# Performance work log

Measured on AMD Instinct MI355X. Metric: run time of the kernel, lower is better.

The kernel has to match this reference:

```python
import jax, jax.numpy as jnp
import numpy as np

N = 50000
E = 1600000
IN_CH = 128
HID = 32
HEADS = 4
OUT_CH = 1
BN_EPS = 1e-5
NEG_SLOPE = 0.2


def _gat_layer(x, src, dst, W, att_src, att_dst, bias, heads, ch, concat, n_nodes):
    # x: [N, F_in], W: [F_in, heads*ch]
    h = (x @ W).reshape(n_nodes, heads, ch)            # [N, H, C]
    e_src = jnp.einsum('nhc,hc->nh', h, att_src)       # [N, H]
    e_dst = jnp.einsum('nhc,hc->nh', h, att_dst)       # [N, H]
    alpha = jax.nn.leaky_relu(e_src[src] + e_dst[dst], NEG_SLOPE)  # [E, H]
    # segment softmax over incoming edges of each dst node
    m = jax.ops.segment_max(alpha, dst, num_segments=n_nodes)      # [N, H]
    ex = jnp.exp(alpha - m[dst])
    den = jax.ops.segment_sum(ex, dst, num_segments=n_nodes)       # [N, H]
    a = ex / (den[dst] + 1e-16)                                    # [E, H]
    out = jax.ops.segment_sum(a[:, :, None] * h[src], dst, num_segments=n_nodes)  # [N, H, C]
    out = out.reshape(n_nodes, heads * ch) if concat else out.mean(axis=1)
    return out + bias


def _batch_norm(x, gamma, beta):
    mean = x.mean(axis=0)
    var = x.var(axis=0)  # biased, as torch uses for normalization
    return (x - mean) * jax.lax.rsqrt(var + BN_EPS) * gamma + beta


def setup_inputs() -> dict:
    key = jax.random.key(0)
    ks = jax.random.split(key, 16)
    hd = HID * HEADS  # 128
    s = lambda fan: 1.0 / np.sqrt(fan)
    return {
        'x': jax.random.normal(ks[0], (N, IN_CH), dtype=jnp.float32),
        'edge_index': jax.random.randint(ks[1], (2, E), 0, N, dtype=jnp.int64),
        'W1': jax.random.normal(ks[2], (IN_CH, hd), dtype=jnp.float32) * s(IN_CH),
        'a1s': jax.random.normal(ks[3], (HEADS, HID), dtype=jnp.float32) * s(HID),
        'a1d': jax.random.normal(ks[4], (HEADS, HID), dtype=jnp.float32) * s(HID),
        'b1': jnp.zeros((hd,), dtype=jnp.float32),
        'g1': jnp.ones((hd,), dtype=jnp.float32),
        'be1': jnp.zeros((hd,), dtype=jnp.float32),
        'W2': jax.random.normal(ks[5], (hd, hd), dtype=jnp.float32) * s(hd),
        'a2s': jax.random.normal(ks[6], (HEADS, HID), dtype=jnp.float32) * s(HID),
        'a2d': jax.random.normal(ks[7], (HEADS, HID), dtype=jnp.float32) * s(HID),
        'b2': jnp.zeros((hd,), dtype=jnp.float32),
        'g2': jnp.ones((hd,), dtype=jnp.float32),
        'be2': jnp.zeros((hd,), dtype=jnp.float32),
        'W3': jax.random.normal(ks[8], (hd, OUT_CH), dtype=jnp.float32) * s(hd),
        'a3s': jax.random.normal(ks[9], (1, OUT_CH), dtype=jnp.float32),
        'a3d': jax.random.normal(ks[10], (1, OUT_CH), dtype=jnp.float32),
        'b3': jnp.zeros((OUT_CH,), dtype=jnp.float32),
    }


def reference(x, edge_index, W1, a1s, a1d, b1, g1, be1, W2, a2s, a2d, b2, g2, be2, W3, a3s, a3d, b3):
    # add self loops (PyG GATConv default), guarantees every dst has >=1 edge
    loops = jnp.arange(N, dtype=edge_index.dtype)
    src = jnp.concatenate([edge_index[0], loops])
    dst = jnp.concatenate([edge_index[1], loops])

    h = _gat_layer(x, src, dst, W1, a1s, a1d, b1, HEADS, HID, True, N)
    h = jax.nn.relu(_batch_norm(h, g1, be1))
    h = _gat_layer(h, src, dst, W2, a2s, a2d, b2, HEADS, HID, True, N)
    h = jax.nn.relu(_batch_norm(h, g2, be2))
    h = _gat_layer(h, src, dst, W3, a3s, a3d, b3, 1, OUT_CH, True, N)
    return jax.nn.relu(h)
```

## Files before the change

### kernel.cpp

```cpp
#include <hip/hip_runtime.h>
#include <hip/hip_fp16.h>
#include <math.h>

#define NEG_SLOPE 0.2f
#define NBMAX 256
#define CHUNK 2048
#define DCAP 16384
#define NREP 32

typedef _Float16 half8 __attribute__((ext_vector_type(8)));
typedef float f32x4 __attribute__((ext_vector_type(4)));

__device__ __forceinline__ float lrelu(float x) { return x > 0.f ? x : NEG_SLOPE * x; }

__device__ __forceinline__ float h2f(unsigned short u) {
    __half h = *(__half*)&u;
    return __half2float(h);
}

__global__ __launch_bounds__(256) void k_hist(const int* __restrict__ ei, int* __restrict__ bCntR,
                                              int E, int n) {
    __shared__ int lh[NBMAX];
    for (int i = threadIdx.x; i < NBMAX; i += 256) lh[i] = 0;
    __syncthreads();
    int E2 = E + n;
    for (int e = blockIdx.x * 256 + threadIdx.x; e < E2; e += gridDim.x * 256) {
        int d = (e < E) ? ei[E + e] : (e - E);
        atomicAdd(&lh[d >> 8], 1);
    }
    __syncthreads();
    int rep = blockIdx.x & (NREP - 1);
    for (int i = threadIdx.x; i < NBMAX; i += 256)
        if (lh[i]) atomicAdd(&bCntR[rep * NBMAX + i], lh[i]);
}

__global__ __launch_bounds__(256) void k_bscan(const int* __restrict__ bCntR, int* __restrict__ bOff,
                                               int* __restrict__ bFill, int* __restrict__ rowptr,
                                               int n, int E2) {
    int NB = (n + 255) >> 8;
    int tid = threadIdx.x, lane = tid & 63, wid = tid >> 6;
    int v0 = 0, v1 = 0, v2 = 0, v3 = 0;
    #pragma unroll
    for (int r = 0; r < NREP; r += 4) {
        v0 += bCntR[(r + 0) * NBMAX + tid];
        v1 += bCntR[(r + 1) * NBMAX + tid];
        v2 += bCntR[(r + 2) * NBMAX + tid];
        v3 += bCntR[(r + 3) * NBMAX + tid];
    }
    int v = (tid < NB) ? (v0 + v1 + v2 + v3) : 0;
    int s = v;
    #pragma unroll
    for (int off = 1; off < 64; off <<= 1) {
        int t = __shfl_up(s, off);
        if (lane >= off) s += t;
    }
    __shared__ int ws[4];
    if (lane == 63) ws[wid] = s;
    __syncthreads();
    if (tid == 0) {
        int c = 0;
        #pragma unroll
        for (int i = 0; i < 4; ++i) { int t = ws[i]; ws[i] = c; c += t; }
    }
    __syncthreads();
    s += ws[wid];
    int excl = s - v;
    if (tid < NB) { bOff[tid] = excl; bFill[tid] = excl; }
    if (tid == NB - 1) bOff[NB] = excl + v;
    if (tid == 0) rowptr[n] = E2;
}

__global__ __launch_bounds__(256) void k_partition(const int* __restrict__ ei, int* __restrict__ bFill,
                                                   unsigned int* __restrict__ staging, int E, int n) {
    __shared__ int lh[NBMAX];
    __shared__ int lbase[NBMAX];
    int E2 = E + n;
    int beg = blockIdx.x * CHUNK;
    int end = min(beg + CHUNK, E2);
    for (int i = threadIdx.x; i < NBMAX; i += 256) lh[i] = 0;
    __syncthreads();
    for (int e = beg + threadIdx.x; e < end; e += 256) {
        int d = (e < E) ? ei[E + e] : (e - E);
        atomicAdd(&lh[d >> 8], 1);
    }
    __syncthreads();
    for (int i = threadIdx.x; i < NBMAX; i += 256) {
        int c = lh[i];
        lbase[i] = c ? atomicAdd(&bFill[i], c) : 0;
        lh[i] = 0;
    }
    __syncthreads();
    for (int e = beg + threadIdx.x; e < end; e += 256) {
        int s, d;
        if (e < E) { s = ei[e]; d = ei[E + e]; } else { s = d = e - E; }
        int b = d >> 8;
        int r = atomicAdd(&lh[b], 1);
        staging[lbase[b] + r] = ((unsigned)s << 8) | (unsigned)(d & 255);
    }
}

__global__ __launch_bounds__(512) void k_emit(const unsigned int* __restrict__ staging,
                                              const int* __restrict__ bOff, int* __restrict__ rowptr,
                                              int* __restrict__ csr, int n) {
    __shared__ int lcnt[NBMAX];
    __shared__ int lscan[NBMAX];
    __shared__ int ws[4];
    __shared__ int sorted[DCAP];
    int b = blockIdx.x;
    int gbase = b << 8;
    int beg = bOff[b], end = bOff[b + 1], m = end - beg;
    int tid = threadIdx.x, lane = tid & 63, wid = tid >> 6;

    if (tid < 256) lcnt[tid] = 0;
    __syncthreads();
    for (int j = tid; j < m; j += 512) atomicAdd(&lcnt[staging[beg + j] & 255], 1);
    __syncthreads();
    int v = 0, s = 0;
    if (tid < 256) {
        v = lcnt[tid];
        s = v;
        #pragma unroll
        for (int off = 1; off < 64; off <<= 1) {
            int t = __shfl_up(s, off);
            if (lane >= off) s += t;
        }
        if (lane == 63) ws[wid] = s;
    }
    __syncthreads();
    if (tid == 0) {
        int c = 0;
        #pragma unroll
        for (int i = 0; i < 4; ++i) { int t = ws[i]; ws[i] = c; c += t; }
    }
    __syncthreads();
    if (tid < 256) {
        int excl = s + ws[wid] - v;
        lscan[tid] = excl;
        lcnt[tid] = 0;
        if (gbase + tid < n) rowptr[gbase + tid] = beg + excl;
    }
    __syncthreads();

    if (m <= DCAP) {
        for (int j = tid; j < m; j += 512) {
            unsigned e = staging[beg + j];
            int ld = e & 255;
            int src = e >> 8;
            int r = atomicAdd(&lcnt[ld], 1);
            sorted[lscan[ld] + r] = src;
        }
        __syncthreads();
        for (int j = tid; j < m; j += 512) csr[beg + j] = sorted[j];
    } else {
        for (int j = tid; j < m; j += 512) {
            unsigned e = staging[beg + j];
            int ld = e & 255;
            int src = e >> 8;
            int r = atomicAdd(&lcnt[ld], 1);
            csr[beg + lscan[ld] + r] = src;
        }
    }
}

__global__ __launch_bounds__(256) void k_gemm_mfma(
    const float* __restrict__ X, const float* __restrict__ W,
    unsigned short* __restrict__ Hout,
    const float* __restrict__ scale, const float* __restrict__ shift,
    const float* __restrict__ as_f, const float* __restrict__ ad_f,
    float* __restrict__ es, float* __restrict__ ed,
    float* __restrict__ bnzero, int n) {
    __shared__ _Float16 WT[128 * 128];
    int tid = threadIdx.x;
    if (blockIdx.x < NREP) bnzero[blockIdx.x * 256 + tid] = 0.f;

    const float4* W4 = (const float4*)W;
    #pragma unroll
    for (int t = 0; t < 16; ++t) {
        int flat = tid + t * 256;
        int k = flat >> 5;
        int n4 = flat & 31;
        float4 wv = W4[flat];
        int nb = n4 * 4;
        #pragma unroll
        for (int i = 0; i < 4; ++i) {
            int nn = nb + i;
            float val = (i == 0) ? wv.x : (i == 1) ? wv.y : (i == 2) ? wv.z : wv.w;
            int byte = nn * 256 + k * 2;
            byte ^= (nn & 7) << 4;
            *(_Float16*)((char*)WT + byte) = (_Float16)val;
        }
    }
    __syncthreads();

    int wid = tid >> 6, lane = tid & 63;
    int l15 = lane & 15, lg = lane >> 4;
    int row0 = blockIdx.x * 64 + wid * 16;
    int myrow = row0 + l15;
    bool rok = myrow < n;

    f32x4 acc[8];
    #pragma unroll
    for (int i = 0; i < 8; ++i) acc[i] = (f32x4){0.f, 0.f, 0.f, 0.f};

    #pragma unroll
    for (int ks = 0; ks < 4; ++ks) {
        int kb = ks * 32 + lg * 8;
        half8 a;
        #pragma unroll
        for (int j = 0; j < 8; ++j) a[j] = (_Float16)0.f;
        if (rok) {
            float4 x0 = *(const float4*)(X + (size_t)myrow * 128 + kb);
            float4 x1 = *(const float4*)(X + (size_t)myrow * 128 + kb + 4);
            if (scale) {
                float4 sc0 = *(const float4*)&scale[kb], sh0 = *(const float4*)&shift[kb];
                float4 sc1 = *(const float4*)&scale[kb + 4], sh1 = *(const float4*)&shift[kb + 4];
                x0.x = fmaxf(x0.x * sc0.x + sh0.x, 0.f);
                x0.y = fmaxf(x0.y * sc0.y + sh0.y, 0.f);
                x0.z = fmaxf(x0.z * sc0.z + sh0.z, 0.f);
                x0.w = fmaxf(x0.w * sc0.w + sh0.w, 0.f);
                x1.x = fmaxf(x1.x * sc1.x + sh1.x, 0.f);
                x1.y = fmaxf(x1.y * sc1.y + sh1.y, 0.f);
                x1.z = fmaxf(x1.z * sc1.z + sh1.z, 0.f);
                x1.w = fmaxf(x1.w * sc1.w + sh1.w, 0.f);
            }
            a[0] = (_Float16)x0.x; a[1] = (_Float16)x0.y;
            a[2] = (_Float16)x0.z; a[3] = (_Float16)x0.w;
            a[4] = (_Float16)x1.x; a[5] = (_Float16)x1.y;
            a[6] = (_Float16)x1.z; a[7] = (_Float16)x1.w;
        }
        #pragma unroll
        for (int nt = 0; nt < 8; ++nt) {
            int nn = nt * 16 + l15;
            int byte = nn * 256 + kb * 2;
            byte ^= (nn & 7) << 4;
            half8 b = *(const half8*)((const char*)WT + byte);
            acc[nt] = __builtin_amdgcn_mfma_f32_16x16x32_f16(a, b, acc[nt], 0, 0, 0);
        }
    }

    #pragma unroll
    for (int nt = 0; nt < 8; ++nt) {
        #pragma unroll
        for (int r = 0; r < 4; ++r) {
            int rr = row0 + lg * 4 + r;
            if (rr < n) {
                _Float16 hv = (_Float16)acc[nt][r];
                Hout[(size_t)rr * 128 + nt * 16 + l15] = *(unsigned short*)&hv;
            }
        }
    }

    float asv[8], adv[8];
    #pragma unroll
    for (int nt = 0; nt < 8; ++nt) {
        asv[nt] = as_f[nt * 16 + l15];
        adv[nt] = ad_f[nt * 16 + l15];
    }
    float ps[4][4], pd[4][4];
    #pragma unroll
    for (int h = 0; h < 4; ++h)
        #pragma unroll
        for (int r = 0; r < 4; ++r) { ps[h][r] = 0.f; pd[h][r] = 0.f; }
    #pragma unroll
    for (int nt = 0; nt < 8; ++nt) {
        int h = nt >> 1;
        #pragma unroll
        for (int r = 0; r < 4; ++r) {
            ps[h][r] += acc[nt][r] * asv[nt];
            pd[h][r] += acc[nt][r] * adv[nt];
        }
    }
    #pragma unroll
    for (int off = 1; off <= 8; off <<= 1) {
        #pragma unroll
        for (int h = 0; h < 4; ++h)
            #pragma unroll
            for (int r = 0; r < 4; ++r) {
                ps[h][r] += __shfl_xor(ps[h][r], off);
                pd[h][r] += __shfl_xor(pd[h][r], off);
            }
    }
    if (l15 == 0) {
        #pragma unroll
        for (int r = 0; r < 4; ++r) {
            int rr = row0 + lg * 4 + r;
            if (rr < n) {
                #pragma unroll
                for (int h = 0; h < 4; ++h) {
                    es[(size_t)rr * 4 + h] = ps[h][r];
                    ed[(size_t)rr * 4 + h] = pd[h][r];
                }
            }
        }
    }
}

__global__ __launch_bounds__(256) void k_node_gat(
    const unsigned short* __restrict__ Hf, const float* __restrict__ es, const float* __restrict__ ed,
    const int* __restrict__ ptr, const int* __restrict__ csr,
    const float* __restrict__ bias, float* __restrict__ out, int n) {
    int nd = blockIdx.x * 4 + (threadIdx.x >> 6);
    if (nd >= n) return;
    int lane = threadIdx.x & 63;
    int cg = lane & 15;
    int slot = lane >> 4;
    int hh = cg >> 2;
    int beg = ptr[nd], deg = ptr[nd + 1] - beg;

    float edn = ed[(unsigned)nd * 4u + hh];
    const uint4* H4 = (const uint4*)Hf;
    const int* cs = csr + beg;

    float a0 = 0.f, a1 = 0.f, a2 = 0.f, a3 = 0.f, a4 = 0.f, a5 = 0.f, a6 = 0.f, a7 = 0.f;
    float den = 0.f;

    int i = slot;
    for (; i + 4 < deg; i += 8) {
        int s0 = cs[i];
        int s1 = cs[i + 4];
        float e0 = es[(unsigned)s0 * 4u + hh];
        float e1 = es[(unsigned)s1 * 4u + hh];
        uint4 p0 = H4[(unsigned)s0 * 16u + cg];
        uint4 p1 = H4[(unsigned)s1 * 16u + cg];
        float w0 = __expf(lrelu(e0 + edn) - 16.f);
        float w1 = __expf(lrelu(e1 + edn) - 16.f);
        den += w0 + w1;
        a0 += w0 * h2f(p0.x & 0xffff) + w1 * h2f(p1.x & 0xffff);
        a1 += w0 * h2f(p0.x >> 16)    + w1 * h2f(p1.x >> 16);
        a2 += w0 * h2f(p0.y & 0xffff) + w1 * h2f(p1.y & 0xffff);
        a3 += w0 * h2f(p0.y >> 16)    + w1 * h2f(p1.y >> 16);
        a4 += w0 * h2f(p0.z & 0xffff) + w1 * h2f(p1.z & 0xffff);
        a5 += w0 * h2f(p0.z >> 16)    + w1 * h2f(p1.z >> 16);
        a6 += w0 * h2f(p0.w & 0xffff) + w1 * h2f(p1.w & 0xffff);
        a7 += w0 * h2f(p0.w >> 16)    + w1 * h2f(p1.w >> 16);
    }
    if (i < deg) {
        int s0 = cs[i];
        float e0 = es[(unsigned)s0 * 4u + hh];
        uint4 p0 = H4[(unsigned)s0 * 16u + cg];
        float w0 = __expf(lrelu(e0 + edn) - 16.f);
        den += w0;
        a0 += w0 * h2f(p0.x & 0xffff);
        a1 += w0 * h2f(p0.x >> 16);
        a2 += w0 * h2f(p0.y & 0xffff);
        a3 += w0 * h2f(p0.y >> 16);
        a4 += w0 * h2f(p0.z & 0xffff);
        a5 += w0 * h2f(p0.z >> 16);
        a6 += w0 * h2f(p0.w & 0xffff);
        a7 += w0 * h2f(p0.w >> 16);
    }

    #pragma unroll
    for (int off = 32; off >= 16; off >>= 1) {
        a0 += __shfl_xor(a0, off); a1 += __shfl_xor(a1, off);
        a2 += __shfl_xor(a2, off); a3 += __shfl_xor(a3, off);
        a4 += __shfl_xor(a4, off); a5 += __shfl_xor(a5, off);
        a6 += __shfl_xor(a6, off); a7 += __shfl_xor(a7, off);
        den += __shfl_xor(den, off);
    }

    if (lane < 16) {
        float inv = 1.f / (den + 1e-16f);
        const float4* bv4 = (const float4*)&bias[cg * 8];
        float4 b0 = bv4[0], b1 = bv4[1];
        float4 o0 = make_float4(a0 * inv + b0.x, a1 * inv + b0.y, a2 * inv + b0.z, a3 * inv + b0.w);
        float4 o1 = make_float4(a4 * inv + b1.x, a5 * inv + b1.y, a6 * inv + b1.z, a7 * inv + b1.w);
        float4* o4 = (float4*)&out[(size_t)nd * 128 + cg * 8];
        o4[0] = o0;
        o4[1] = o1;
    }
}

__global__ __launch_bounds__(256) void k_bn_stats(const float* __restrict__ G, float* __restrict__ bnG,
                                                  int n) {
    int tid = threadIdx.x;
    int cg = tid & 31;
    int rsub = tid >> 5;
    const float4* G4 = (const float4*)G;
    float4 s = make_float4(0.f, 0.f, 0.f, 0.f);
    float4 q = make_float4(0.f, 0.f, 0.f, 0.f);
    for (int r = blockIdx.x * 8 + rsub; r < n; r += gridDim.x * 8) {
        float4 v = G4[(size_t)r * 32 + cg];
        s.x += v.x; s.y += v.y; s.z += v.z; s.w += v.w;
        q.x += v.x * v.x; q.y += v.y * v.y; q.z += v.z * v.z; q.w += v.w * v.w;
    }
    s.x += __shfl_xor(s.x, 32); s.y += __shfl_xor(s.y, 32);
    s.z += __shfl_xor(s.z, 32); s.w += __shfl_xor(s.w, 32);
    q.x += __shfl_xor(q.x, 32); q.y += __shfl_xor(q.y, 32);
    q.z += __shfl_xor(q.z, 32); q.w += __shfl_xor(q.w, 32);
    __shared__ float4 redS[4][32];
    __shared__ float4 redQ[4][32];
    int wid = tid >> 6, lane = tid & 63;
    if (lane < 32) { redS[wid][cg] = s; redQ[wid][cg] = q; }
    __syncthreads();
    if (tid < 32) {
        float4 S = redS[0][tid], Q = redQ[0][tid];
        #pragma unroll
        for (int w = 1; w < 4; ++w) {
            float4 a = redS[w][tid], b = redQ[w][tid];
            S.x += a.x; S.y += a.y; S.z += a.z; S.w += a.w;
            Q.x += b.x; Q.y += b.y; Q.z += b.z; Q.w += b.w;
        }
        float* dst = bnG + (blockIdx.x & (NREP - 1)) * 256;
        int c = tid * 4;
        atomicAdd(&dst[c + 0], S.x); atomicAdd(&dst[c + 1], S.y);
        atomicAdd(&dst[c + 2], S.z); atomicAdd(&dst[c + 3], S.w);
        atomicAdd(&dst[128 + c + 0], Q.x); atomicAdd(&dst[128 + c + 1], Q.y);
        atomicAdd(&dst[128 + c + 2], Q.z); atomicAdd(&dst[128 + c + 3], Q.w);
    }
}

__global__ void k_bn_finalize(const float* __restrict__ bnG,
                              const float* __restrict__ g, const float* __restrict__ be,
                              float* __restrict__ scale, float* __restrict__ shift, int n) {
    int c = threadIdx.x;
    float s0 = 0.f, s1 = 0.f, s2 = 0.f, s3 = 0.f;
    float q0 = 0.f, q1 = 0.f, q2 = 0.f, q3 = 0.f;
    #pragma unroll
    for (int r = 0; r < NREP; r += 4) {
        s0 += bnG[(r + 0) * 256 + c];
        s1 += bnG[(r + 1) * 256 + c];
        s2 += bnG[(r + 2) * 256 + c];
        s3 += bnG[(r + 3) * 256 + c];
        q0 += bnG[(r + 0) * 256 + 128 + c];
        q1 += bnG[(r + 1) * 256 + 128 + c];
        q2 += bnG[(r + 2) * 256 + 128 + c];
        q3 += bnG[(r + 3) * 256 + 128 + c];
    }
    float s = (s0 + s1) + (s2 + s3);
    float q = (q0 + q1) + (q2 + q3);
    float mean = s / (float)n;
    float var = q / (float)n - mean * mean;
    float sc = g[c] * rsqrtf(var + 1e-5f);
    scale[c] = sc;
    shift[c] = be[c] - mean * sc;
}

__global__ __launch_bounds__(256) void k_dot3(const float* __restrict__ F, const float* __restrict__ W3,
                                              const float* __restrict__ scale, const float* __restrict__ shift,
                                              float* __restrict__ h3, int n) {
    int wid = threadIdx.x >> 6, lane = threadIdx.x & 63;
    int nd = blockIdx.x * 4 + wid;
    if (nd >= n) return;
    const float* row = F + (size_t)nd * 128;
    float v0 = fmaxf(row[lane] * scale[lane] + shift[lane], 0.f);
    float v1 = fmaxf(row[lane + 64] * scale[lane + 64] + shift[lane + 64], 0.f);
    float v = v0 * W3[lane] + v1 * W3[lane + 64];
    #pragma unroll
    for (int off = 32; off > 0; off >>= 1) v += __shfl_xor(v, off);
    if (lane == 0) h3[nd] = v;
}

__global__ __launch_bounds__(256) void k_gat3(const float* __restrict__ h3, const float* __restrict__ a3s,
                                              const float* __restrict__ a3d, const float* __restrict__ b3,
                                              const int* __restrict__ ptr, const int* __restrict__ csr,
                                              float* __restrict__ out, int n) {
    int nd = blockIdx.x * 4 + (threadIdx.x >> 6);
    if (nd >= n) return;
    int lane = threadIdx.x & 63;
    int beg = ptr[nd], deg = ptr[nd + 1] - beg;
    float As = a3s[0], Ad = a3d[0], B = b3[0];
    float hd = h3[nd] * Ad;
    float den = 0.f, num = 0.f;
    for (int i = lane; i < deg; i += 64) {
        float hs = h3[csr[beg + i]];
        float a = lrelu(hs * As + hd);
        float ex = __expf(a - 16.f);
        den += ex;
        num += ex * hs;
    }
    #pragma unroll
    for (int off = 32; off > 0; off >>= 1) {
        den += __shfl_xor(den, off);
        num += __shfl_xor(num, off);
    }
    if (lane == 0) out[nd] = fmaxf(num / (den + 1e-16f) + B, 0.f);
}

extern "C" void kernel_launch(void* const* d_in, const int* in_sizes, int n_in,
                              void* d_out, int out_size, void* d_ws, size_t ws_size,
                              hipStream_t stream) {
    const int N_ = in_sizes[0] / 128;
    const int E_ = in_sizes[1] / 2;
    const int E2 = E_ + N_;
    const int NB = (N_ + 255) >> 8;

    const float* x = (const float*)d_in[0];
    const int* ei = (const int*)d_in[1];
    const float* W1 = (const float*)d_in[2];
    const float* a1s = (const float*)d_in[3];
    const float* a1d = (const float*)d_in[4];
    const float* b1 = (const float*)d_in[5];
    const float* g1 = (const float*)d_in[6];
    const float* be1 = (const float*)d_in[7];
    const float* W2 = (const float*)d_in[8];
    const float* a2s = (const float*)d_in[9];
    const float* a2d = (const float*)d_in[10];
    const float* b2 = (const float*)d_in[11];
    const float* g2 = (const float*)d_in[12];
    const float* be2 = (const float*)d_in[13];
    const float* W3 = (const float*)d_in[14];
    const float* a3s = (const float*)d_in[15];
    const float* a3d = (const float*)d_in[16];
    const float* b3 = (const float*)d_in[17];
    float* out = (float*)d_out;

    char* p = (char*)d_ws;
    auto alloc = [&](size_t bytes) {
        void* r = (void*)p;
        p += (bytes + 255) & ~(size_t)255;
        return r;
    };
    int* bCntR = (int*)alloc((size_t)NREP * NBMAX * 4);
    int* bOff = (int*)alloc((size_t)(NBMAX + 1) * 4);
    int* bFill = (int*)alloc((size_t)NBMAX * 4);
    int* rowptr = (int*)alloc((size_t)(N_ + 1) * 4);
    unsigned int* staging = (unsigned int*)alloc((size_t)E2 * 4);
    int* csr = (int*)alloc((size_t)E2 * 4);
    unsigned short* Hb = (unsigned short*)alloc((size_t)N_ * 128 * 2);
    float* G = (float*)alloc((size_t)N_ * 128 * 4);
    float* es = (float*)alloc((size_t)N_ * 4 * 4);
    float* ed = (float*)alloc((size_t)N_ * 4 * 4);
    float* h3 = (float*)alloc((size_t)N_ * 4);
    float* bnG = (float*)alloc((size_t)NREP * 256 * 4);
    float* bnss = (float*)alloc(256 * 4);

    hipMemsetAsync(bCntR, 0, (size_t)NREP * NBMAX * 4, stream);
    k_hist<<<512, 256, 0, stream>>>(ei, bCntR, E_, N_);
    k_bscan<<<1, 256, 0, stream>>>(bCntR, bOff, bFill, rowptr, N_, E2);
    k_partition<<<(E2 + CHUNK - 1) / CHUNK, 256, 0, stream>>>(ei, bFill, staging, E_, N_);
    k_emit<<<NB, 512, 0, stream>>>(staging, bOff, rowptr, csr, N_);

    int gemmB = (N_ + 63) / 64;
    int gatB = (N_ + 3) / 4;

    k_gemm_mfma<<<gemmB, 256, 0, stream>>>(x, W1, Hb, nullptr, nullptr, a1s, a1d, es, ed, bnG, N_);
    k_node_gat<<<gatB, 256, 0, stream>>>(Hb, es, ed, rowptr, csr, b1, G, N_);
    k_bn_stats<<<512, 256, 0, stream>>>(G, bnG, N_);
    k_bn_finalize<<<1, 128, 0, stream>>>(bnG, g1, be1, bnss, bnss + 128, N_);

    k_gemm_mfma<<<gemmB, 256, 0, stream>>>(G, W2, Hb, bnss, bnss + 128, a2s, a2d, es, ed, bnG, N_);
    k_node_gat<<<gatB, 256, 0, stream>>>(Hb, es, ed, rowptr, csr, b2, G, N_);
    k_bn_stats<<<512, 256, 0, stream>>>(G, bnG, N_);
    k_bn_finalize<<<1, 128, 0, stream>>>(bnG, g2, be2, bnss, bnss + 128, N_);

    k_dot3<<<(N_ + 3) / 4, 256, 0, stream>>>(G, W3, bnss, bnss + 128, h3, N_);
    k_gat3<<<gatB, 256, 0, stream>>>(h3, a3s, a3d, b3, rowptr, csr, out, N_);
}
```

Measured before the change: 267.0 us.

## Pre-swizzle weights once, fold BN finalize into stats kernel, enlarge partition chunk

Adds a small kernel that converts W1 and W2 to swizzled fp16 once, so each GEMM block copies ready-made data into LDS instead of converting fp32 weights itself. The separate BN finalize kernels are dropped: the last block of k_bn_stats, found through an atomic counter, computes scale and shift. CHUNK for edge partitioning is doubled. The aim is fewer kernel launches and less redundant per-block weight conversion, in exchange for one extra launch and a threadfence and last-block pattern.

```diff
diff --git a/kernel.cpp b/kernel.cpp
--- a/kernel.cpp
+++ b/kernel.cpp
@@ -4,7 +4,7 @@
 
 #define NEG_SLOPE 0.2f
 #define NBMAX 256
-#define CHUNK 2048
+#define CHUNK 4096
 #define DCAP 16384
 #define NREP 32
 
@@ -162,8 +162,21 @@
     }
 }
 
+__global__ __launch_bounds__(256) void k_wprep(const float* __restrict__ W1, const float* __restrict__ W2,
+                                               unsigned short* __restrict__ Wsw) {
+    int flat = blockIdx.x * 256 + threadIdx.x;
+    int layer = flat >> 14;
+    int idx = flat & 16383;
+    int k = idx >> 7, nn = idx & 127;
+    const float* W = layer ? W2 : W1;
+    _Float16 h = (_Float16)W[idx];
+    int byte = nn * 256 + k * 2;
+    byte ^= (nn & 7) << 4;
+    *(unsigned short*)((char*)(Wsw + (size_t)layer * 16384) + byte) = *(unsigned short*)&h;
+}
+
 __global__ __launch_bounds__(256) void k_gemm_mfma(
-    const float* __restrict__ X, const float* __restrict__ W,
+    const float* __restrict__ X, const unsigned short* __restrict__ Wsw,
     unsigned short* __restrict__ Hout,
     const float* __restrict__ scale, const float* __restrict__ shift,
     const float* __restrict__ as_f, const float* __restrict__ ad_f,
@@ -173,23 +186,10 @@
     int tid = threadIdx.x;
     if (blockIdx.x < NREP) bnzero[blockIdx.x * 256 + tid] = 0.f;
 
-    const float4* W4 = (const float4*)W;
-    #pragma unroll
-    for (int t = 0; t < 16; ++t) {
-        int flat = tid + t * 256;
-        int k = flat >> 5;
-        int n4 = flat & 31;
-        float4 wv = W4[flat];
-        int nb = n4 * 4;
-        #pragma unroll
-        for (int i = 0; i < 4; ++i) {
-            int nn = nb + i;
-            float val = (i == 0) ? wv.x : (i == 1) ? wv.y : (i == 2) ? wv.z : wv.w;
-            int byte = nn * 256 + k * 2;
-            byte ^= (nn & 7) << 4;
-            *(_Float16*)((char*)WT + byte) = (_Float16)val;
-        }
-    }
+    const uint4* Wg = (const uint4*)Wsw;
+    uint4* WT4 = (uint4*)WT;
+    #pragma unroll
+    for (int t = 0; t < 8; ++t) WT4[tid + t * 256] = Wg[tid + t * 256];
     __syncthreads();
 
     int wid = tid >> 6, lane = tid & 63;
@@ -372,6 +372,9 @@
 }
 
 __global__ __launch_bounds__(256) void k_bn_stats(const float* __restrict__ G, float* __restrict__ bnG,
+                                                  int* __restrict__ cnt,
+                                                  const float* __restrict__ g, const float* __restrict__ be,
+                                                  float* __restrict__ scale, float* __restrict__ shift,
                                                   int n) {
     int tid = threadIdx.x;
     int cg = tid & 31;
@@ -390,6 +393,7 @@
     q.z += __shfl_xor(q.z, 32); q.w += __shfl_xor(q.w, 32);
     __shared__ float4 redS[4][32];
     __shared__ float4 redQ[4][32];
+    __shared__ int isLast;
     int wid = tid >> 6, lane = tid & 63;
     if (lane < 32) { redS[wid][cg] = s; redQ[wid][cg] = q; }
     __syncthreads();
@@ -408,32 +412,39 @@
         atomicAdd(&dst[128 + c + 0], Q.x); atomicAdd(&dst[128 + c + 1], Q.y);
         atomicAdd(&dst[128 + c + 2], Q.z); atomicAdd(&dst[128 + c + 3], Q.w);
     }
-}
-
-__global__ void k_bn_finalize(const float* __restrict__ bnG,
-                              const float* __restrict__ g, const float* __restrict__ be,
-                              float* __restrict__ scale, float* __restrict__ shift, int n) {
-    int c = threadIdx.x;
-    float s0 = 0.f, s1 = 0.f, s2 = 0.f, s3 = 0.f;
-    float q0 = 0.f, q1 = 0.f, q2 = 0.f, q3 = 0.f;
-    #pragma unroll
-    for (int r = 0; r < NREP; r += 4) {
-        s0 += bnG[(r + 0) * 256 + c];
-        s1 += bnG[(r + 1) * 256 + c];
-        s2 += bnG[(r + 2) * 256 + c];
-        s3 += bnG[(r + 3) * 256 + c];
-        q0 += bnG[(r + 0) * 256 + 128 + c];
-        q1 += bnG[(r + 1) * 256 + 128 + c];
-        q2 += bnG[(r + 2) * 256 + 128 + c];
-        q3 += bnG[(r + 3) * 256 + 128 + c];
-    }
-    float s = (s0 + s1) + (s2 + s3);
-    float q = (q0 + q1) + (q2 + q3);
-    float mean = s / (float)n;
-    float var = q / (float)n - mean * mean;
-    float sc = g[c] * rsqrtf(var + 1e-5f);
-    scale[c] = sc;
-    shift[c] = be[c] - mean * sc;
+    __syncthreads();
+    if (tid == 0) {
+        __threadfence();
+        int old = atomicAdd(cnt, 1);
+        isLast = (old == (int)gridDim.x - 1) ? 1 : 0;
+    }
+    __syncthreads();
+    if (isLast) {
+        __threadfence();
+        if (tid < 128) {
+            const volatile float* vb = bnG;
+            float s0 = 0.f, s1 = 0.f, s2 = 0.f, s3 = 0.f;
+            float q0 = 0.f, q1 = 0.f, q2 = 0.f, q3 = 0.f;
+            #pragma unroll
+            for (int r = 0; r < NREP; r += 4) {
+                s0 += vb[(r + 0) * 256 + tid];
+                s1 += vb[(r + 1) * 256 + tid];
+                s2 += vb[(r + 2) * 256 + tid];
+                s3 += vb[(r + 3) * 256 + tid];
+                q0 += vb[(r + 0) * 256 + 128 + tid];
+                q1 += vb[(r + 1) * 256 + 128 + tid];
+                q2 += vb[(r + 2) * 256 + 128 + tid];
+                q3 += vb[(r + 3) * 256 + 128 + tid];
+            }
+            float ss = (s0 + s1) + (s2 + s3);
+            float qq = (q0 + q1) + (q2 + q3);
+            float mean = ss / (float)n;
+            float var = qq / (float)n - mean * mean;
+            float sc = g[tid] * rsqrtf(var + 1e-5f);
+            scale[tid] = sc;
+            shift[tid] = be[tid] - mean * sc;
+        }
+    }
 }
 
 __global__ __launch_bounds__(256) void k_dot3(const float* __restrict__ F, const float* __restrict__ W3,
@@ -512,6 +523,7 @@
         return r;
     };
     int* bCntR = (int*)alloc((size_t)NREP * NBMAX * 4);
+    int* lbc = (int*)alloc(8);
     int* bOff = (int*)alloc((size_t)(NBMAX + 1) * 4);
     int* bFill = (int*)alloc((size_t)NBMAX * 4);
     int* rowptr = (int*)alloc((size_t)(N_ + 1) * 4);
@@ -522,10 +534,12 @@
     float* es = (float*)alloc((size_t)N_ * 4 * 4);
     float* ed = (float*)alloc((size_t)N_ * 4 * 4);
     float* h3 = (float*)alloc((size_t)N_ * 4);
+    unsigned short* Wsw = (unsigned short*)alloc((size_t)2 * 16384 * 2);
     float* bnG = (float*)alloc((size_t)NREP * 256 * 4);
     float* bnss = (float*)alloc(256 * 4);
 
-    hipMemsetAsync(bCntR, 0, (size_t)NREP * NBMAX * 4, stream);
+    hipMemsetAsync(bCntR, 0, (size_t)NREP * NBMAX * 4 + 256, stream);
+    k_wprep<<<128, 256, 0, stream>>>(W1, W2, Wsw);
     k_hist<<<512, 256, 0, stream>>>(ei, bCntR, E_, N_);
     k_bscan<<<1, 256, 0, stream>>>(bCntR, bOff, bFill, rowptr, N_, E2);
     k_partition<<<(E2 + CHUNK - 1) / CHUNK, 256, 0, stream>>>(ei, bFill, staging, E_, N_);
@@ -534,15 +548,13 @@
     int gemmB = (N_ + 63) / 64;
     int gatB = (N_ + 3) / 4;
 
-    k_gemm_mfma<<<gemmB, 256, 0, stream>>>(x, W1, Hb, nullptr, nullptr, a1s, a1d, es, ed, bnG, N_);
+    k_gemm_mfma<<<gemmB, 256, 0, stream>>>(x, Wsw, Hb, nullptr, nullptr, a1s, a1d, es, ed, bnG, N_);
     k_node_gat<<<gatB, 256, 0, stream>>>(Hb, es, ed, rowptr, csr, b1, G, N_);
-    k_bn_stats<<<512, 256, 0, stream>>>(G, bnG, N_);
-    k_bn_finalize<<<1, 128, 0, stream>>>(bnG, g1, be1, bnss, bnss + 128, N_);
-
-    k_gemm_mfma<<<gemmB, 256, 0, stream>>>(G, W2, Hb, bnss, bnss + 128, a2s, a2d, es, ed, bnG, N_);
+    k_bn_stats<<<512, 256, 0, stream>>>(G, bnG, lbc, g1, be1, bnss, bnss + 128, N_);
+
+    k_gemm_mfma<<<gemmB, 256, 0, stream>>>(G, Wsw + 16384, Hb, bnss, bnss + 128, a2s, a2d, es, ed, bnG, N_);
     k_node_gat<<<gatB, 256, 0, stream>>>(Hb, es, ed, rowptr, csr, b2, G, N_);
-    k_bn_stats<<<512, 256, 0, stream>>>(G, bnG, N_);
-    k_bn_finalize<<<1, 128, 0, stream>>>(bnG, g2, be2, bnss, bnss + 128, N_);
+    k_bn_stats<<<512, 256, 0, stream>>>(G, bnG, lbc + 1, g2, be2, bnss, bnss + 128, N_);
 
     k_dot3<<<(N_ + 3) / 4, 256, 0, stream>>>(G, W3, bnss, bnss + 128, h3, N_);
     k_gat3<<<gatB, 256, 0, stream>>>(h3, a3s, a3d, b3, rowptr, csr, out, N_);
```

New measurement: 282.4 us. 1.06x slower.
